# Performance work log

Measured on AMD Instinct MI355X. Metric: run time of the kernel, lower is better.

## Reference

```python
import jax, jax.numpy as jnp
import numpy as np

D_INNER = 2048
STATE_DIM = 16
DT_MIN = 1e-4


def _softplus(x):
    return jnp.log1p(jnp.exp(-jnp.abs(x))) + jnp.maximum(x, 0)


def setup_inputs() -> dict:
    key = jax.random.key(0)
    ks = jax.random.split(key, 11)
    B, L, d, N = 4, 4096, D_INNER, STATE_DIM
    u = jax.random.normal(ks[0], (B, L, d), dtype=jnp.float32)
    s = 0.02
    return {
        "u": u,
        "Wdt": jax.random.normal(ks[1], (d, d), jnp.float32) / jnp.sqrt(d),
        "bdt": jnp.zeros((d,), jnp.float32),
        "Wb": jax.random.normal(ks[2], (d, d), jnp.float32) / jnp.sqrt(d),
        "bb": jnp.zeros((d,), jnp.float32),
        "Wc": jax.random.normal(ks[3], (d, d), jnp.float32) / jnp.sqrt(d),
        "bc": jnp.zeros((d,), jnp.float32),
        "a_raw": s * jax.random.normal(ks[4], (d, N), jnp.float32),
        "B_base": s * jax.random.normal(ks[5], (d, N), jnp.float32),
        "C_base": s * jax.random.normal(ks[6], (d, N), jnp.float32),
        "D": jnp.zeros((d,), jnp.float32),
    }


def reference(u, Wdt, bdt, Wb, bb, Wc, bc, a_raw, B_base, C_base, D):
    # u: (B, L, d_inner)
    B, L, d = u.shape
    N = a_raw.shape[1]
    A = -_softplus(a_raw)  # (d, N), stable diagonal
    # Input-dependent projections, computed once over the whole sequence
    dt = _softplus(jnp.einsum("bld,de->ble", u, Wdt) + bdt) + DT_MIN  # dt_scale=1.0
    b_t = jnp.einsum("bld,de->ble", u, Wb) + bb
    c_t = jnp.einsum("bld,de->ble", u, Wc) + bc

    def step(x, inp):
        u_s, dt_s, b_s, c_s = inp  # each (B, d)
        Abar = jnp.exp(dt_s[:, :, None] * A)                     # (B, d, N)
        Bbar = dt_s[:, :, None] * (b_s[:, :, None] * B_base)    # (B, d, N)
        x = Abar * x + Bbar * u_s[:, :, None]                    # (B, d, N)
        y = jnp.sum(c_s[:, :, None] * C_base * x, axis=-1) + D * u_s
        return x, y

    carry0 = jnp.zeros((B, d, N), dtype=u.dtype)
    xs = (
        jnp.swapaxes(u, 0, 1),
        jnp.swapaxes(dt, 0, 1),
        jnp.swapaxes(b_t, 0, 1),
        jnp.swapaxes(c_t, 0, 1),
    )
    carry_out, ys = jax.lax.scan(step, carry0, xs)
    y = jnp.swapaxes(ys, 0, 1)  # (B, L, d)
    return carry_out, y
```

## Files before the change

kernel.cpp:

```cpp
#include <hip/hip_runtime.h>
#include <cstdint>
#include <cstddef>

#define D_IN   2048
#define STATE_N 16
#define SEQ_L  4096
#define BATCH  4
#define M_TOT  (BATCH * SEQ_L)
#define NCAT   (3 * D_IN)
#define LC     128
#define NCHUNK (SEQ_L / LC)
#define BDN    (BATCH * D_IN * STATE_N)
#define BD     (BATCH * D_IN)

#define BK     32

typedef __bf16 bf16x8 __attribute__((ext_vector_type(8)));
typedef float  f32x4  __attribute__((ext_vector_type(4)));
typedef unsigned int u32x4 __attribute__((ext_vector_type(4)));

__device__ __forceinline__ float softplus_f(float x) {
    return log1pf(expf(-fabsf(x))) + fmaxf(x, 0.f);
}
__device__ __forceinline__ unsigned short f2bf(float f) {
    unsigned u = __float_as_uint(f);
    u += 0x7FFFu + ((u >> 16) & 1u);
    return (unsigned short)(u >> 16);
}
__device__ __forceinline__ float bf2f(unsigned short h) {
    return __uint_as_float(((unsigned)h) << 16);
}

__device__ __forceinline__ void gload_lds16(const unsigned short* g, unsigned short* l) {
    __builtin_amdgcn_global_load_lds(
        (const __attribute__((address_space(1))) unsigned int*)(const void*)g,
        (__attribute__((address_space(3))) unsigned int*)(void*)l,
        16, 0, 0);
}

__global__ __launch_bounds__(256) void k_cvt_u(const float* __restrict__ u,
                                               unsigned short* __restrict__ ub) {
    size_t i = ((size_t)blockIdx.x * 256 + threadIdx.x) * 8;
    f32x4 a = *(const f32x4*)(u + i);
    f32x4 b = *(const f32x4*)(u + i + 4);
    u32x4 o;
    o[0] = (unsigned)f2bf(a[0]) | ((unsigned)f2bf(a[1]) << 16);
    o[1] = (unsigned)f2bf(a[2]) | ((unsigned)f2bf(a[3]) << 16);
    o[2] = (unsigned)f2bf(b[0]) | ((unsigned)f2bf(b[1]) << 16);
    o[3] = (unsigned)f2bf(b[2]) | ((unsigned)f2bf(b[3]) << 16);
    *(u32x4*)(ub + i) = o;
}

__global__ __launch_bounds__(256) void k_transpose(const float* __restrict__ Wdt,
                                                   const float* __restrict__ Wb,
                                                   const float* __restrict__ Wc,
                                                   unsigned short* __restrict__ Btb) {
    __shared__ float tile[32][33];
    int e0 = blockIdx.x * 32;
    int k0 = blockIdx.y * 32;
    const float* W; int eo;
    if (e0 >= 2 * D_IN)      { W = Wc; eo = e0 - 2 * D_IN; }
    else if (e0 >= D_IN)     { W = Wb; eo = e0 - D_IN; }
    else                     { W = Wdt; eo = e0; }
    int tx = threadIdx.x, ty = threadIdx.y;
#pragma unroll
    for (int i = ty; i < 32; i += 8)
        tile[i][tx] = W[(size_t)(k0 + i) * D_IN + eo + tx];
    __syncthreads();
#pragma unroll
    for (int i = ty; i < 32; i += 8)
        Btb[(size_t)(e0 + i) * D_IN + k0 + tx] = f2bf(tile[tx][i]);
}

__global__ __launch_bounds__(256) void k_gemm(const unsigned short* __restrict__ Au,
                                              const unsigned short* __restrict__ Btb,
                                              const float* __restrict__ bdt,
                                              const float* __restrict__ bbv,
                                              const float* __restrict__ bcv,
                                              unsigned short* __restrict__ dtp,
                                              unsigned short* __restrict__ btp,
                                              unsigned short* __restrict__ ctp) {
    __shared__ unsigned short As[128 * BK];
    __shared__ unsigned short Bs[128 * BK];

    int tid = threadIdx.x;
    int lane = tid & 63, wave = tid >> 6;
    int wr = wave >> 1, wc = wave & 1;
    int l15 = lane & 15, lhi = lane >> 4;

    int flat = blockIdx.x;
    int bm = flat / 48, bn = flat % 48;

    const unsigned short* Ag = Au + (size_t)(bm * 128) * D_IN;
    const unsigned short* Bg = Btb + (size_t)(bn * 128) * D_IN;

    f32x4 acc[4][4] = {};

    const int s0 = tid, s1 = 256 + tid;
    const int r0 = s0 >> 2, r1 = s1 >> 2;
    const size_t ga0 = (size_t)r0 * D_IN + (((s0 & 3) ^ ((r0 >> 1) & 3)) * 8);
    const size_t ga1 = (size_t)r1 * D_IN + (((s1 & 3) ^ ((r1 >> 1) & 3)) * 8);

    const int swzr = (lhi ^ ((l15 >> 1) & 3)) * 8;
    const int aoff = (wr * 64 + l15) * BK + swzr;
    const int boff = (wc * 64 + l15) * BK + swzr;

    for (int kt = 0; kt < D_IN; kt += BK) {
        __syncthreads();
        gload_lds16(Ag + kt + ga0, &As[s0 * 8]);
        gload_lds16(Ag + kt + ga1, &As[s1 * 8]);
        gload_lds16(Bg + kt + ga0, &Bs[s0 * 8]);
        gload_lds16(Bg + kt + ga1, &Bs[s1 * 8]);
        __syncthreads();
        bf16x8 af[4], bfr[4];
#pragma unroll
        for (int i = 0; i < 4; ++i)
            af[i] = *(const bf16x8*)&As[aoff + i * 16 * BK];
#pragma unroll
        for (int j = 0; j < 4; ++j)
            bfr[j] = *(const bf16x8*)&Bs[boff + j * 16 * BK];
#pragma unroll
        for (int i = 0; i < 4; ++i)
#pragma unroll
            for (int j = 0; j < 4; ++j)
                acc[i][j] = __builtin_amdgcn_mfma_f32_16x16x32_bf16(af[i], bfr[j], acc[i][j], 0, 0, 0);
    }

    int gm0 = bm * 128 + wr * 64 + lhi * 4;
    int col0 = (bn & 15) * 128 + wc * 64 + l15;
    int region = bn >> 4;
    unsigned short* outp = (region == 0) ? dtp : (region == 1) ? btp : ctp;
    const float* biasp = (region == 0) ? bdt : (region == 1) ? bbv : bcv;
#pragma unroll
    for (int j = 0; j < 4; ++j) {
        int col = col0 + j * 16;
        float bias = biasp[col];
#pragma unroll
        for (int i = 0; i < 4; ++i)
#pragma unroll
            for (int r = 0; r < 4; ++r) {
                float v = acc[i][j][r] + bias;
                if (region == 0) v = softplus_f(v) + 1e-4f;
                outp[(size_t)(gm0 + i * 16 + r) * D_IN + col] = f2bf(v);
            }
    }
}

__device__ __forceinline__ void loadA8(const unsigned short* __restrict__ ub,
                                       const unsigned short* __restrict__ dtp,
                                       const unsigned short* __restrict__ btp,
                                       size_t base, int l0,
                                       float (&T)[8], float (&U)[8], float (&Bv)[8]) {
#pragma unroll
    for (int i = 0; i < 8; ++i) {
        size_t off = base + (size_t)(l0 + i) * D_IN;
        T[i] = bf2f(dtp[off]);
        U[i] = bf2f(ub[off]);
        Bv[i] = bf2f(btp[off]);
    }
}

__device__ __forceinline__ void compA8(float (&x)[16], float& sdt,
                                       const float (&A2)[16], const float (&Bb)[16],
                                       const float (&T)[8], const float (&U)[8],
                                       const float (&Bv)[8]) {
#pragma unroll
    for (int i = 0; i < 8; ++i) {
        float dtv = T[i];
        float s = dtv * Bv[i] * U[i];
        sdt += dtv;
#pragma unroll
        for (int n = 0; n < 16; ++n)
            x[n] = fmaf(exp2f(A2[n] * dtv), x[n], s * Bb[n]);
    }
}

__global__ __launch_bounds__(256) void k_scanA(const unsigned short* __restrict__ ub,
                                               const unsigned short* __restrict__ dtp,
                                               const unsigned short* __restrict__ btp,
                                               const float* __restrict__ a_raw,
                                               const float* __restrict__ Bbp,
                                               float* __restrict__ localx,
                                               float* __restrict__ sumdt) {
    int tid = threadIdx.x;
    int d = blockIdx.x * 256 + tid;
    int c = blockIdx.y, b = blockIdx.z;
    const float L2E = 1.4426950408889634f;

    float A2[16], Bb[16];
#pragma unroll
    for (int n = 0; n < 16; n += 4) {
        f32x4 a = *(const f32x4*)(a_raw + d * STATE_N + n);
        f32x4 bv = *(const f32x4*)(Bbp + d * STATE_N + n);
#pragma unroll
        for (int j = 0; j < 4; ++j) {
            A2[n + j] = -softplus_f(a[j]) * L2E;
            Bb[n + j] = bv[j];
        }
    }

    size_t base = ((size_t)b * SEQ_L + (size_t)c * LC) * D_IN + d;
    float x[16];
#pragma unroll
    for (int n = 0; n < 16; ++n) x[n] = 0.f;
    float sdt = 0.f;

    float tA[8], uA[8], bA[8], tB[8], uB[8], bB[8];
    loadA8(ub, dtp, btp, base, 0, tA, uA, bA);
    for (int l0 = 0; l0 < LC; l0 += 16) {
        loadA8(ub, dtp, btp, base, l0 + 8, tB, uB, bB);
        compA8(x, sdt, A2, Bb, tA, uA, bA);
        if (l0 + 16 < LC)
            loadA8(ub, dtp, btp, base, l0 + 16, tA, uA, bA);
        compA8(x, sdt, A2, Bb, tB, uB, bB);
    }

    size_t sb = (size_t)c * BDN + ((size_t)b * D_IN + d) * STATE_N;
#pragma unroll
    for (int n = 0; n < 16; n += 4) {
        f32x4 v; v[0] = x[n]; v[1] = x[n + 1]; v[2] = x[n + 2]; v[3] = x[n + 3];
        *(f32x4*)(localx + sb + n) = v;
    }
    sumdt[(size_t)c * BD + (size_t)b * D_IN + d] = sdt;
}

__global__ __launch_bounds__(256) void k_scanB(const float* __restrict__ localx,
                                               const float* __restrict__ sumdt,
                                               const float* __restrict__ a_raw,
                                               float* __restrict__ x0,
                                               float* __restrict__ carry) {
    int gid = blockIdx.x * 256 + threadIdx.x;
    int n = gid & 15;
    int d = (gid >> 4) & (D_IN - 1);
    int bd = gid >> 4;
    float A2 = -softplus_f(a_raw[d * STATE_N + n]) * 1.4426950408889634f;
    float x = 0.f;
    for (int c = 0; c < NCHUNK; ++c) {
        x0[(size_t)c * BDN + gid] = x;
        float sdt = sumdt[(size_t)c * BD + bd];
        x = fmaf(exp2f(A2 * sdt), x, localx[(size_t)c * BDN + gid]);
    }
    carry[gid] = x;
}

__device__ __forceinline__ void loadC8(const unsigned short* __restrict__ ub,
                                       const unsigned short* __restrict__ dtp,
                                       const unsigned short* __restrict__ btp,
                                       const unsigned short* __restrict__ ctp,
                                       size_t base, int l0,
                                       float (&T)[8], float (&U)[8],
                                       float (&Bv)[8], float (&Cv)[8]) {
#pragma unroll
    for (int i = 0; i < 8; ++i) {
        size_t off = base + (size_t)(l0 + i) * D_IN;
        T[i] = bf2f(dtp[off]);
        U[i] = bf2f(ub[off]);
        Bv[i] = bf2f(btp[off]);
        Cv[i] = bf2f(ctp[off]);
    }
}

__device__ __forceinline__ void compC8(float (&x)[16],
                                       const float (&A2)[16], const float (&Bb)[16],
                                       const float (&Cb)[16], float Dd,
                                       float* __restrict__ y, size_t base, int l0,
                                       const float (&T)[8], const float (&U)[8],
                                       const float (&Bv)[8], const float (&Cv)[8]) {
#pragma unroll
    for (int i = 0; i < 8; ++i) {
        float dtv = T[i], uv = U[i];
        float s = dtv * Bv[i] * uv;
        float y0 = 0.f, y1 = 0.f, y2 = 0.f, y3 = 0.f;
#pragma unroll
        for (int n = 0; n < 16; n += 4) {
            x[n]     = fmaf(exp2f(A2[n] * dtv),     x[n],     s * Bb[n]);
            y0 = fmaf(Cb[n], x[n], y0);
            x[n + 1] = fmaf(exp2f(A2[n + 1] * dtv), x[n + 1], s * Bb[n + 1]);
            y1 = fmaf(Cb[n + 1], x[n + 1], y1);
            x[n + 2] = fmaf(exp2f(A2[n + 2] * dtv), x[n + 2], s * Bb[n + 2]);
            y2 = fmaf(Cb[n + 2], x[n + 2], y2);
            x[n + 3] = fmaf(exp2f(A2[n + 3] * dtv), x[n + 3], s * Bb[n + 3]);
            y3 = fmaf(Cb[n + 3], x[n + 3], y3);
        }
        y[base + (size_t)(l0 + i) * D_IN] = fmaf(Dd, uv, Cv[i] * ((y0 + y1) + (y2 + y3)));
    }
}

__global__ __launch_bounds__(256) void k_scanC(const unsigned short* __restrict__ ub,
                                               const unsigned short* __restrict__ dtp,
                                               const unsigned short* __restrict__ btp,
                                               const unsigned short* __restrict__ ctp,
                                               const float* __restrict__ a_raw,
                                               const float* __restrict__ Bbp,
                                               const float* __restrict__ Cbp,
                                               const float* __restrict__ Dv,
                                               const float* __restrict__ x0,
                                               float* __restrict__ y) {
    int tid = threadIdx.x;
    int d = blockIdx.x * 256 + tid;
    int c = blockIdx.y, b = blockIdx.z;
    const float L2E = 1.4426950408889634f;

    float A2[16], Bb[16], Cb[16];
#pragma unroll
    for (int n = 0; n < 16; n += 4) {
        f32x4 a = *(const f32x4*)(a_raw + d * STATE_N + n);
        f32x4 bv = *(const f32x4*)(Bbp + d * STATE_N + n);
        f32x4 cv = *(const f32x4*)(Cbp + d * STATE_N + n);
#pragma unroll
        for (int j = 0; j < 4; ++j) {
            A2[n + j] = -softplus_f(a[j]) * L2E;
            Bb[n + j] = bv[j];
            Cb[n + j] = cv[j];
        }
    }
    float Dd = Dv[d];

    float x[16];
    size_t xb = (size_t)c * BDN + ((size_t)b * D_IN + d) * STATE_N;
#pragma unroll
    for (int n = 0; n < 16; n += 4) {
        f32x4 v = *(const f32x4*)(x0 + xb + n);
        x[n] = v[0]; x[n + 1] = v[1]; x[n + 2] = v[2]; x[n + 3] = v[3];
    }

    size_t base = ((size_t)b * SEQ_L + (size_t)c * LC) * D_IN + d;
    float tA[8], uA[8], bA[8], cA[8], tB[8], uB[8], bB[8], cB[8];
    loadC8(ub, dtp, btp, ctp, base, 0, tA, uA, bA, cA);
    for (int l0 = 0; l0 < LC; l0 += 16) {
        loadC8(ub, dtp, btp, ctp, base, l0 + 8, tB, uB, bB, cB);
        compC8(x, A2, Bb, Cb, Dd, y, base, l0, tA, uA, bA, cA);
        if (l0 + 16 < LC)
            loadC8(ub, dtp, btp, ctp, base, l0 + 16, tA, uA, bA, cA);
        compC8(x, A2, Bb, Cb, Dd, y, base, l0 + 8, tB, uB, bB, cB);
    }
}

extern "C" void kernel_launch(void* const* d_in, const int* in_sizes, int n_in,
                              void* d_out, int out_size, void* d_ws, size_t ws_size,
                              hipStream_t stream) {
    const float* u     = (const float*)d_in[0];
    const float* Wdt   = (const float*)d_in[1];
    const float* bdt   = (const float*)d_in[2];
    const float* Wb    = (const float*)d_in[3];
    const float* bb    = (const float*)d_in[4];
    const float* Wc    = (const float*)d_in[5];
    const float* bc    = (const float*)d_in[6];
    const float* a_raw = (const float*)d_in[7];
    const float* Bbp   = (const float*)d_in[8];
    const float* Cbp   = (const float*)d_in[9];
    const float* Dv    = (const float*)d_in[10];

    float* out = (float*)d_out;
    float* carry = out;
    float* y = out + (size_t)BATCH * D_IN * STATE_N;

    const size_t Mel = (size_t)M_TOT * D_IN;
    char* ws = (char*)d_ws;
    unsigned short* ub  = (unsigned short*)ws;
    unsigned short* Btb = (unsigned short*)(ws + Mel * 2);
    char* p = ws + Mel * 2 + (size_t)NCAT * D_IN * 2;
    unsigned short* dtp = (unsigned short*)p;
    unsigned short* btp = (unsigned short*)(p + Mel * 2);
    unsigned short* ctp = (unsigned short*)(p + Mel * 4);
    char* q = p + Mel * 6;
    float* localx = (float*)q;
    float* x0v    = (float*)(q + (size_t)NCHUNK * BDN * 4);
    float* sumdt  = (float*)(q + (size_t)NCHUNK * BDN * 8);

    k_cvt_u<<<dim3((M_TOT * D_IN) / (256 * 8)), dim3(256), 0, stream>>>(u, ub);
    k_transpose<<<dim3(NCAT / 32, D_IN / 32), dim3(32, 8), 0, stream>>>(Wdt, Wb, Wc, Btb);
    k_gemm<<<dim3((M_TOT / 128) * (NCAT / 128)), dim3(256), 0, stream>>>(ub, Btb, bdt, bb, bc,
                                                                         dtp, btp, ctp);
    k_scanA<<<dim3(D_IN / 256, NCHUNK, BATCH), dim3(256), 0, stream>>>(ub, dtp, btp, a_raw,
                                                                       Bbp, localx, sumdt);
    k_scanB<<<dim3(BDN / 256), dim3(256), 0, stream>>>(localx, sumdt, a_raw, x0v, carry);
    k_scanC<<<dim3(D_IN / 256, NCHUNK, BATCH), dim3(256), 0, stream>>>(ub, dtp, btp, ctp,
                                                                       a_raw, Bbp, Cbp, Dv,
                                                                       x0v, y);
}
```

Before: 1.139 ms.

## Store projections and u transposed so scan threads read contiguous time vectors

The GEMM epilogue now writes dt, b and c in a d-major (transposed) layout, and the u conversion kernel also emits a transposed bf16 copy. The scan kernels can then load 8 consecutive timesteps per thread with one 16-byte vector load instead of 8 strided scalar loads. Chunk length is halved to raise the number of parallel blocks. The cost is an extra transposed u buffer and write traffic, plus GEMM stores that are now strided across columns. Halving the chunk length also doubles the intermediate state buffers and the serial work in scanB.

```diff
diff --git a/kernel.cpp b/kernel.cpp
--- a/kernel.cpp
+++ b/kernel.cpp
@@ -8,7 +8,7 @@
 #define BATCH  4
 #define M_TOT  (BATCH * SEQ_L)
 #define NCAT   (3 * D_IN)
-#define LC     128
+#define LC     64
 #define NCHUNK (SEQ_L / LC)
 #define BDN    (BATCH * D_IN * STATE_N)
 #define BD     (BATCH * D_IN)
@@ -18,6 +18,8 @@
 typedef __bf16 bf16x8 __attribute__((ext_vector_type(8)));
 typedef float  f32x4  __attribute__((ext_vector_type(4)));
 typedef unsigned int u32x4 __attribute__((ext_vector_type(4)));
+typedef unsigned short u16x8 __attribute__((ext_vector_type(8)));
+typedef unsigned short u16x4 __attribute__((ext_vector_type(4)));
 
 __device__ __forceinline__ float softplus_f(float x) {
     return log1pf(expf(-fabsf(x))) + fmaxf(x, 0.f);
@@ -38,17 +40,23 @@
         16, 0, 0);
 }
 
-__global__ __launch_bounds__(256) void k_cvt_u(const float* __restrict__ u,
-                                               unsigned short* __restrict__ ub) {
-    size_t i = ((size_t)blockIdx.x * 256 + threadIdx.x) * 8;
-    f32x4 a = *(const f32x4*)(u + i);
-    f32x4 b = *(const f32x4*)(u + i + 4);
-    u32x4 o;
-    o[0] = (unsigned)f2bf(a[0]) | ((unsigned)f2bf(a[1]) << 16);
-    o[1] = (unsigned)f2bf(a[2]) | ((unsigned)f2bf(a[3]) << 16);
-    o[2] = (unsigned)f2bf(b[0]) | ((unsigned)f2bf(b[1]) << 16);
-    o[3] = (unsigned)f2bf(b[2]) | ((unsigned)f2bf(b[3]) << 16);
-    *(u32x4*)(ub + i) = o;
+__global__ __launch_bounds__(256) void k_cvt_u_t(const float* __restrict__ u,
+                                                 unsigned short* __restrict__ ub,
+                                                 unsigned short* __restrict__ uT) {
+    __shared__ float tile[32][33];
+    int m0 = blockIdx.x * 32;
+    int d0 = blockIdx.y * 32;
+    int tx = threadIdx.x, ty = threadIdx.y;
+#pragma unroll
+    for (int i = ty; i < 32; i += 8) {
+        float v = u[(size_t)(m0 + i) * D_IN + d0 + tx];
+        tile[i][tx] = v;
+        ub[(size_t)(m0 + i) * D_IN + d0 + tx] = f2bf(v);
+    }
+    __syncthreads();
+#pragma unroll
+    for (int i = ty; i < 32; i += 8)
+        uT[(size_t)(d0 + i) * M_TOT + m0 + tx] = f2bf(tile[tx][i]);
 }
 
 __global__ __launch_bounds__(256) void k_transpose(const float* __restrict__ Wdt,
@@ -136,38 +144,26 @@
         int col = col0 + j * 16;
         float bias = biasp[col];
 #pragma unroll
-        for (int i = 0; i < 4; ++i)
+        for (int i = 0; i < 4; ++i) {
+            u16x4 w;
 #pragma unroll
             for (int r = 0; r < 4; ++r) {
                 float v = acc[i][j][r] + bias;
                 if (region == 0) v = softplus_f(v) + 1e-4f;
-                outp[(size_t)(gm0 + i * 16 + r) * D_IN + col] = f2bf(v);
+                w[r] = f2bf(v);
             }
-    }
-}
-
-__device__ __forceinline__ void loadA8(const unsigned short* __restrict__ ub,
-                                       const unsigned short* __restrict__ dtp,
-                                       const unsigned short* __restrict__ btp,
-                                       size_t base, int l0,
-                                       float (&T)[8], float (&U)[8], float (&Bv)[8]) {
+            *(u16x4*)&outp[(size_t)col * M_TOT + gm0 + i * 16] = w;
+        }
+    }
+}
+
+__device__ __forceinline__ void compA8T(float (&x)[16], float& sdt,
+                                        const float (&A2)[16], const float (&Bb)[16],
+                                        const u16x8& T, const u16x8& U, const u16x8& Bv) {
 #pragma unroll
     for (int i = 0; i < 8; ++i) {
-        size_t off = base + (size_t)(l0 + i) * D_IN;
-        T[i] = bf2f(dtp[off]);
-        U[i] = bf2f(ub[off]);
-        Bv[i] = bf2f(btp[off]);
-    }
-}
-
-__device__ __forceinline__ void compA8(float (&x)[16], float& sdt,
-                                       const float (&A2)[16], const float (&Bb)[16],
-                                       const float (&T)[8], const float (&U)[8],
-                                       const float (&Bv)[8]) {
-#pragma unroll
-    for (int i = 0; i < 8; ++i) {
-        float dtv = T[i];
-        float s = dtv * Bv[i] * U[i];
+        float dtv = bf2f(T[i]);
+        float s = dtv * bf2f(Bv[i]) * bf2f(U[i]);
         sdt += dtv;
 #pragma unroll
         for (int n = 0; n < 16; ++n)
@@ -175,7 +171,7 @@
     }
 }
 
-__global__ __launch_bounds__(256) void k_scanA(const unsigned short* __restrict__ ub,
+__global__ __launch_bounds__(256) void k_scanA(const unsigned short* __restrict__ uT,
                                                const unsigned short* __restrict__ dtp,
                                                const unsigned short* __restrict__ btp,
                                                const float* __restrict__ a_raw,
@@ -199,20 +195,25 @@
         }
     }
 
-    size_t base = ((size_t)b * SEQ_L + (size_t)c * LC) * D_IN + d;
+    size_t base = (size_t)d * M_TOT + (size_t)b * SEQ_L + (size_t)c * LC;
     float x[16];
 #pragma unroll
     for (int n = 0; n < 16; ++n) x[n] = 0.f;
     float sdt = 0.f;
 
-    float tA[8], uA[8], bA[8], tB[8], uB[8], bB[8];
-    loadA8(ub, dtp, btp, base, 0, tA, uA, bA);
+    u16x8 tA, uA, bA, tB, uB, bB;
+    tA = *(const u16x8*)&dtp[base]; uA = *(const u16x8*)&uT[base]; bA = *(const u16x8*)&btp[base];
     for (int l0 = 0; l0 < LC; l0 += 16) {
-        loadA8(ub, dtp, btp, base, l0 + 8, tB, uB, bB);
-        compA8(x, sdt, A2, Bb, tA, uA, bA);
-        if (l0 + 16 < LC)
-            loadA8(ub, dtp, btp, base, l0 + 16, tA, uA, bA);
-        compA8(x, sdt, A2, Bb, tB, uB, bB);
+        tB = *(const u16x8*)&dtp[base + l0 + 8];
+        uB = *(const u16x8*)&uT[base + l0 + 8];
+        bB = *(const u16x8*)&btp[base + l0 + 8];
+        compA8T(x, sdt, A2, Bb, tA, uA, bA);
+        if (l0 + 16 < LC) {
+            tA = *(const u16x8*)&dtp[base + l0 + 16];
+            uA = *(const u16x8*)&uT[base + l0 + 16];
+            bA = *(const u16x8*)&btp[base + l0 + 16];
+        }
+        compA8T(x, sdt, A2, Bb, tB, uB, bB);
     }
 
     size_t sb = (size_t)c * BDN + ((size_t)b * D_IN + d) * STATE_N;
@@ -243,33 +244,16 @@
     carry[gid] = x;
 }
 
-__device__ __forceinline__ void loadC8(const unsigned short* __restrict__ ub,
-                                       const unsigned short* __restrict__ dtp,
-                                       const unsigned short* __restrict__ btp,
-                                       const unsigned short* __restrict__ ctp,
-                                       size_t base, int l0,
-                                       float (&T)[8], float (&U)[8],
-                                       float (&Bv)[8], float (&Cv)[8]) {
+__device__ __forceinline__ void compC8T(float (&x)[16],
+                                        const float (&A2)[16], const float (&Bb)[16],
+                                        const float (&Cb)[16], float Dd,
+                                        float* __restrict__ y, size_t yb, int l0,
+                                        const u16x8& T, const u16x8& U,
+                                        const u16x8& Bv, const u16x8& Cv) {
 #pragma unroll
     for (int i = 0; i < 8; ++i) {
-        size_t off = base + (size_t)(l0 + i) * D_IN;
-        T[i] = bf2f(dtp[off]);
-        U[i] = bf2f(ub[off]);
-        Bv[i] = bf2f(btp[off]);
-        Cv[i] = bf2f(ctp[off]);
-    }
-}
-
-__device__ __forceinline__ void compC8(float (&x)[16],
-                                       const float (&A2)[16], const float (&Bb)[16],
-                                       const float (&Cb)[16], float Dd,
-                                       float* __restrict__ y, size_t base, int l0,
-                                       const float (&T)[8], const float (&U)[8],
-                                       const float (&Bv)[8], const float (&Cv)[8]) {
-#pragma unroll
-    for (int i = 0; i < 8; ++i) {
-        float dtv = T[i], uv = U[i];
-        float s = dtv * Bv[i] * uv;
+        float dtv = bf2f(T[i]), uv = bf2f(U[i]);
+        float s = dtv * bf2f(Bv[i]) * uv;
         float y0 = 0.f, y1 = 0.f, y2 = 0.f, y3 = 0.f;
 #pragma unroll
         for (int n = 0; n < 16; n += 4) {
@@ -282,11 +266,11 @@
             x[n + 3] = fmaf(exp2f(A2[n + 3] * dtv), x[n + 3], s * Bb[n + 3]);
             y3 = fmaf(Cb[n + 3], x[n + 3], y3);
         }
-        y[base + (size_t)(l0 + i) * D_IN] = fmaf(Dd, uv, Cv[i] * ((y0 + y1) + (y2 + y3)));
-    }
-}
-
-__global__ __launch_bounds__(256) void k_scanC(const unsigned short* __restrict__ ub,
+        y[yb + (size_t)(l0 + i) * D_IN] = fmaf(Dd, uv, bf2f(Cv[i]) * ((y0 + y1) + (y2 + y3)));
+    }
+}
+
+__global__ __launch_bounds__(256) void k_scanC(const unsigned short* __restrict__ uT,
                                                const unsigned short* __restrict__ dtp,
                                                const unsigned short* __restrict__ btp,
                                                const unsigned short* __restrict__ ctp,
@@ -324,15 +308,25 @@
         x[n] = v[0]; x[n + 1] = v[1]; x[n + 2] = v[2]; x[n + 3] = v[3];
     }
 
-    size_t base = ((size_t)b * SEQ_L + (size_t)c * LC) * D_IN + d;
-    float tA[8], uA[8], bA[8], cA[8], tB[8], uB[8], bB[8], cB[8];
-    loadC8(ub, dtp, btp, ctp, base, 0, tA, uA, bA, cA);
+    size_t base = (size_t)d * M_TOT + (size_t)b * SEQ_L + (size_t)c * LC;
+    size_t yb = ((size_t)b * SEQ_L + (size_t)c * LC) * D_IN + d;
+
+    u16x8 tA, uA, bA, cA, tB, uB, bB, cB;
+    tA = *(const u16x8*)&dtp[base]; uA = *(const u16x8*)&uT[base];
+    bA = *(const u16x8*)&btp[base]; cA = *(const u16x8*)&ctp[base];
     for (int l0 = 0; l0 < LC; l0 += 16) {
-        loadC8(ub, dtp, btp, ctp, base, l0 + 8, tB, uB, bB, cB);
-        compC8(x, A2, Bb, Cb, Dd, y, base, l0, tA, uA, bA, cA);
-        if (l0 + 16 < LC)
-            loadC8(ub, dtp, btp, ctp, base, l0 + 16, tA, uA, bA, cA);
-        compC8(x, A2, Bb, Cb, Dd, y, base, l0 + 8, tB, uB, bB, cB);
+        tB = *(const u16x8*)&dtp[base + l0 + 8];
+        uB = *(const u16x8*)&uT[base + l0 + 8];
+        bB = *(const u16x8*)&btp[base + l0 + 8];
+        cB = *(const u16x8*)&ctp[base + l0 + 8];
+        compC8T(x, A2, Bb, Cb, Dd, y, yb, l0, tA, uA, bA, cA);
+        if (l0 + 16 < LC) {
+            tA = *(const u16x8*)&dtp[base + l0 + 16];
+            uA = *(const u16x8*)&uT[base + l0 + 16];
+            bA = *(const u16x8*)&btp[base + l0 + 16];
+            cA = *(const u16x8*)&ctp[base + l0 + 16];
+        }
+        compC8T(x, A2, Bb, Cb, Dd, y, yb, l0 + 8, tB, uB, bB, cB);
     }
 }
 
@@ -358,8 +352,9 @@
     const size_t Mel = (size_t)M_TOT * D_IN;
     char* ws = (char*)d_ws;
     unsigned short* ub  = (unsigned short*)ws;
-    unsigned short* Btb = (unsigned short*)(ws + Mel * 2);
-    char* p = ws + Mel * 2 + (size_t)NCAT * D_IN * 2;
+    unsigned short* uT  = (unsigned short*)(ws + Mel * 2);
+    unsigned short* Btb = (unsigned short*)(ws + Mel * 4);
+    char* p = ws + Mel * 4 + (size_t)NCAT * D_IN * 2;
     unsigned short* dtp = (unsigned short*)p;
     unsigned short* btp = (unsigned short*)(p + Mel * 2);
     unsigned short* ctp = (unsigned short*)(p + Mel * 4);
@@ -368,14 +363,14 @@
     float* x0v    = (float*)(q + (size_t)NCHUNK * BDN * 4);
     float* sumdt  = (float*)(q + (size_t)NCHUNK * BDN * 8);
 
-    k_cvt_u<<<dim3((M_TOT * D_IN) / (256 * 8)), dim3(256), 0, stream>>>(u, ub);
+    k_cvt_u_t<<<dim3(M_TOT / 32, D_IN / 32), dim3(32, 8), 0, stream>>>(u, ub, uT);
     k_transpose<<<dim3(NCAT / 32, D_IN / 32), dim3(32, 8), 0, stream>>>(Wdt, Wb, Wc, Btb);
     k_gemm<<<dim3((M_TOT / 128) * (NCAT / 128)), dim3(256), 0, stream>>>(ub, Btb, bdt, bb, bc,
                                                                          dtp, btp, ctp);
-    k_scanA<<<dim3(D_IN / 256, NCHUNK, BATCH), dim3(256), 0, stream>>>(ub, dtp, btp, a_raw,
+    k_scanA<<<dim3(D_IN / 256, NCHUNK, BATCH), dim3(256), 0, stream>>>(uT, dtp, btp, a_raw,
                                                                        Bbp, localx, sumdt);
     k_scanB<<<dim3(BDN / 256), dim3(256), 0, stream>>>(localx, sumdt, a_raw, x0v, carry);
-    k_scanC<<<dim3(D_IN / 256, NCHUNK, BATCH), dim3(256), 0, stream>>>(ub, dtp, btp, ctp,
+    k_scanC<<<dim3(D_IN / 256, NCHUNK, BATCH), dim3(256), 0, stream>>>(uT, dtp, btp, ctp,
                                                                        a_raw, Bbp, Cbp, Dv,
                                                                        x0v, y);
 }
```

New measurement: 1.191 ms. +4.6%, slower.
